# Performance work log

Measured on AMD Instinct MI355X. Metric: run time of the kernel, lower is better.

The kernel has to match this reference:

```python
import jax, jax.numpy as jnp
import numpy as np

HEADS = 12
HEAD_SIZE = 64
NEG = 1e12


def setup_inputs() -> dict:
    key = jax.random.key(0)
    k1, k2 = jax.random.split(key)
    B, L, D = 32, 512, 768
    x = jax.random.normal(k1, (B, L, D), dtype=jnp.float32)
    mask = jnp.ones((B, L), dtype=jnp.float32)  # padding mask (1 = valid)
    W = jax.random.normal(k2, (D, HEADS * HEAD_SIZE * 2), dtype=jnp.float32) * 0.02
    b = jnp.zeros((HEADS * HEAD_SIZE * 2,), dtype=jnp.float32)
    return {"x": x, "mask": mask, "W": W, "b": b}


def _rope_sin_cos(L, s, dtype):
    # bert4keras SinusoidalPositionEmbedding: pe[..., ::2] = sin, pe[..., 1::2] = cos
    pos = jnp.arange(L, dtype=dtype)
    freq = jnp.power(10000.0, -2.0 * jnp.arange(s // 2, dtype=dtype) / s)
    ang = pos[:, None] * freq[None, :]            # [L, s/2]
    sin = jnp.repeat(jnp.sin(ang), 2, axis=-1)    # [L, s]
    cos = jnp.repeat(jnp.cos(ang), 2, axis=-1)    # [L, s]
    return sin, cos


def _rotate_half(t):
    # interleaved rotation: (-t1, t0, -t3, t2, ...)
    t2 = jnp.stack([-t[..., 1::2], t[..., ::2]], axis=-1)
    return t2.reshape(t.shape)


def reference(x, mask, W, b):
    B, L, D = x.shape
    s = HEAD_SIZE
    proj = x @ W + b                               # [B, L, heads*2s]
    proj = proj.reshape(B, L, HEADS, 2 * s)        # split-into-heads + stack
    qw, kw = proj[..., :s], proj[..., s:]
    sin, cos = _rope_sin_cos(L, s, x.dtype)
    sin = sin[None, :, None, :]                    # [1, L, 1, s]
    cos = cos[None, :, None, :]
    qw = qw * cos + _rotate_half(qw) * sin
    kw = kw * cos + _rotate_half(kw) * sin
    logits = jnp.einsum('bmhs,bnhs->bhmn', qw, kw)  # [B, H, L, L]
    m2 = mask[:, None, :, None]
    m3 = mask[:, None, None, :]
    logits = logits * m2 + (1.0 - m2) * -NEG
    logits = logits * m3 + (1.0 - m3) * -NEG
    tril = jnp.tril(jnp.ones((L, L), dtype=logits.dtype), -1)  # strictly lower
    logits = logits - tril * NEG                    # keep upper-triangular spans
    return (logits / jnp.sqrt(jnp.asarray(s, logits.dtype))).reshape(B, HEADS, L * L)
```

## Files before the change

### kernel.cpp

```cpp
#include <hip/hip_runtime.h>
#include <hip/hip_bf16.h>

#define HEADS 12
#define HSIZE 64
#define BATCH 32
#define SEQ 512
#define DIM 768
#define NOUT 1536
#define MROWS 16384
#define NEGV 1e12f

typedef __bf16 bf16x8 __attribute__((ext_vector_type(8)));
typedef float f32x4 __attribute__((ext_vector_type(4)));
typedef unsigned short u16x8 __attribute__((ext_vector_type(8)));
typedef unsigned short u16x4 __attribute__((ext_vector_type(4)));

__device__ __forceinline__ void async16(const void* g, void* l) {
  __builtin_amdgcn_global_load_lds(
      (const __attribute__((address_space(1))) void*)g,
      (__attribute__((address_space(3))) void*)l, 16, 0, 0);
}

__device__ __forceinline__ unsigned short f2b(float f) {
  union { __hip_bfloat16 h; unsigned short u; } cv;
  cv.h = __float2bfloat16(f);
  return cv.u;
}

__global__ void rope_table(float* __restrict__ sin_t, float* __restrict__ cos_t) {
  int idx = blockIdx.x * 256 + threadIdx.x;
  if (idx < SEQ * 32) {
    int pos = idx >> 5;
    int i = idx & 31;
    float freq = powf(10000.0f, -2.0f * (float)i / 64.0f);
    float ang = (float)pos * freq;
    sin_t[idx] = sinf(ang);
    cos_t[idx] = cosf(ang);
  }
}

__global__ void convert_x(const float* __restrict__ x, unsigned short* __restrict__ xb) {
  int idx = blockIdx.x * 256 + threadIdx.x;
  float4 v = ((const float4*)x)[idx];
  ushort4 o;
  o.x = f2b(v.x); o.y = f2b(v.y); o.z = f2b(v.z); o.w = f2b(v.w);
  ((ushort4*)xb)[idx] = o;
}

__global__ void transpose_w(const float* __restrict__ W, unsigned short* __restrict__ Wt) {
  __shared__ unsigned short tile[32][33];
  int n0 = blockIdx.x * 32;
  int k0 = blockIdx.y * 32;
  int tx = threadIdx.x & 31, ty = threadIdx.x >> 5;
#pragma unroll
  for (int j = 0; j < 32; j += 8) {
    tile[ty + j][tx] = f2b(W[(size_t)(k0 + ty + j) * NOUT + n0 + tx]);
  }
  __syncthreads();
#pragma unroll
  for (int j = 0; j < 32; j += 8) {
    Wt[(size_t)(n0 + ty + j) * DIM + k0 + tx] = tile[tx][ty + j];
  }
}

__global__ __launch_bounds__(256) void gemm_rope(
    const unsigned short* __restrict__ xb, const unsigned short* __restrict__ wt,
    const float* __restrict__ bias, const float* __restrict__ sin_t,
    const float* __restrict__ cos_t, unsigned short* __restrict__ q_ws,
    unsigned short* __restrict__ k_ws) {
  __shared__ __align__(16) unsigned short smem[128 * 136];
  unsigned short* As = smem;
  unsigned short* Bs = smem + 4096;
  const int tid = threadIdx.x;
  const int bx = blockIdx.x;
  const int tn = (bx % (NOUT / 128)) * 128;
  const int tm = (bx / (NOUT / 128)) * 128;
  const int wid = tid >> 6, lane = tid & 63;
  const int wm = (wid >> 1) * 64, wn = (wid & 1) * 64;
  const int lrow = lane & 15, lk = (lane >> 4) * 8;

  const int sr = tid >> 2;
  const int sc = (tid & 3) * 8;
  const unsigned short* a_src0 = xb + (size_t)(tm + sr) * DIM + sc;
  const unsigned short* a_src1 = xb + (size_t)(tm + 64 + sr) * DIM + sc;
  const unsigned short* b_src0 = wt + (size_t)(tn + sr) * DIM + sc;
  const unsigned short* b_src1 = wt + (size_t)(tn + 64 + sr) * DIM + sc;
  unsigned short* a_dst0 = &As[tid * 8];
  unsigned short* a_dst1 = &As[2048 + tid * 8];
  unsigned short* b_dst0 = &Bs[tid * 8];
  unsigned short* b_dst1 = &Bs[2048 + tid * 8];

  f32x4 acc[4][4] = {};
  for (int k0 = 0; k0 < DIM; k0 += 32) {
    async16(a_src0 + k0, a_dst0);
    async16(a_src1 + k0, a_dst1);
    async16(b_src0 + k0, b_dst0);
    async16(b_src1 + k0, b_dst1);
    __syncthreads();
    bf16x8 nf[4], mf[4];
#pragma unroll
    for (int i = 0; i < 4; ++i) {
      nf[i] = *(const bf16x8*)&Bs[(wn + i * 16 + lrow) * 32 + lk];
      mf[i] = *(const bf16x8*)&As[(wm + i * 16 + lrow) * 32 + lk];
    }
#pragma unroll
    for (int ai = 0; ai < 4; ++ai)
#pragma unroll
      for (int bi = 0; bi < 4; ++bi)
        acc[ai][bi] = __builtin_amdgcn_mfma_f32_16x16x32_bf16(
            nf[ai], mf[bi], acc[ai][bi], 0, 0, 0);
    __syncthreads();
  }

#pragma unroll
  for (int ai = 0; ai < 4; ++ai) {
    const int nloc = wn + ai * 16 + (lane >> 4) * 4;
    const int colb = tn + nloc;
    const int d0 = colb & 63;
    const float4 b4 = *(const float4*)&bias[colb];
#pragma unroll
    for (int bi = 0; bi < 4; ++bi) {
      const int mloc = wm + bi * 16 + lrow;
      const int pos = (tm + mloc) & (SEQ - 1);
      const float2 s01 = *(const float2*)&sin_t[pos * 32 + (d0 >> 1)];
      const float2 c01 = *(const float2*)&cos_t[pos * 32 + (d0 >> 1)];
      const float v0 = acc[ai][bi][0] + b4.x;
      const float v1 = acc[ai][bi][1] + b4.y;
      const float v2 = acc[ai][bi][2] + b4.z;
      const float v3 = acc[ai][bi][3] + b4.w;
      u16x4 pk;
      pk[0] = f2b(fmaf(v0, c01.x, -v1 * s01.x));
      pk[1] = f2b(fmaf(v1, c01.x,  v0 * s01.x));
      pk[2] = f2b(fmaf(v2, c01.y, -v3 * s01.y));
      pk[3] = f2b(fmaf(v3, c01.y,  v2 * s01.y));
      *(u16x4*)&smem[mloc * 136 + nloc] = pk;
    }
  }
  __syncthreads();

  const int bq = tm >> 9;
  const int pos0 = tm & (SEQ - 1);
  const int head = tn >> 7;
  const size_t rowbase = ((size_t)(bq * HEADS + head) * SEQ + pos0);
  const int rr = tid >> 3;
  const int cc = tid & 7;
#pragma unroll
  for (int p = 0; p < 4; ++p) {
    const int r = p * 32 + rr;
    u16x8 vq = *(const u16x8*)&smem[r * 136 + cc * 8];
    u16x8 vk = *(const u16x8*)&smem[r * 136 + 64 + cc * 8];
    *(u16x8*)&q_ws[(rowbase + r) * 64 + cc * 8] = vq;
    *(u16x8*)&k_ws[(rowbase + r) * 64 + cc * 8] = vk;
  }
}

__global__ __launch_bounds__(256) void qk_kernel(
    const unsigned short* __restrict__ q_ws, const unsigned short* __restrict__ k_ws,
    const float* __restrict__ mask, float* __restrict__ out) {
  __shared__ __align__(16) float ot[128 * 132];
  const int bx = blockIdx.x;
  const int bh = bx >> 4;
  const int t = bx & 15;
  const int tmm = (t >> 2) * 128, tnn = (t & 3) * 128;
  const int bidx = bh / HEADS;
  const int tid = threadIdx.x, wid = tid >> 6, lane = tid & 63;
  const int wm = (wid >> 1) * 64, wn = (wid & 1) * 64;
  const int lrow = lane & 15, lk = (lane >> 4) * 8;
  const unsigned short* Q = q_ws + ((size_t)bh << 15);
  const unsigned short* K = k_ws + ((size_t)bh << 15);

  bf16x8 kf[4][2], qf[4][2];
#pragma unroll
  for (int i = 0; i < 4; ++i) {
#pragma unroll
    for (int ks = 0; ks < 2; ++ks) {
      kf[i][ks] = *(const bf16x8*)&K[(size_t)(tnn + wn + i * 16 + lrow) * 64 + ks * 32 + lk];
      qf[i][ks] = *(const bf16x8*)&Q[(size_t)(tmm + wm + i * 16 + lrow) * 64 + ks * 32 + lk];
    }
  }
  f32x4 acc[4][4] = {};
#pragma unroll
  for (int ai = 0; ai < 4; ++ai)
#pragma unroll
    for (int bi = 0; bi < 4; ++bi) {
      acc[ai][bi] = __builtin_amdgcn_mfma_f32_16x16x32_bf16(kf[ai][0], qf[bi][0], acc[ai][bi], 0, 0, 0);
      acc[ai][bi] = __builtin_amdgcn_mfma_f32_16x16x32_bf16(kf[ai][1], qf[bi][1], acc[ai][bi], 0, 0, 0);
    }

#pragma unroll
  for (int ai = 0; ai < 4; ++ai) {
    const int nloc = wn + ai * 16 + (lane >> 4) * 4;
#pragma unroll
    for (int bi = 0; bi < 4; ++bi) {
      const int mloc = wm + bi * 16 + lrow;
      *(f32x4*)&ot[mloc * 132 + nloc] = acc[ai][bi];
    }
  }
  __syncthreads();

  float* obase = out + ((size_t)bh << 18);
  const float* mrow = mask + (size_t)bidx * SEQ;
  const int cc = tid & 31;
  const int rr = tid >> 5;
  const int n0 = tnn + cc * 4;
  const f32x4 m3v = *(const f32x4*)&mrow[n0];
#pragma unroll
  for (int p = 0; p < 16; ++p) {
    const int r = p * 8 + rr;
    const int m = tmm + r;
    f32x4 v = *(const f32x4*)&ot[r * 132 + cc * 4];
    const float m2 = mrow[m];
    f32x4 o;
#pragma unroll
    for (int j = 0; j < 4; ++j) {
      float vv = v[j];
      vv = vv * m2 + (1.0f - m2) * (-NEGV);
      vv = vv * m3v[j] + (1.0f - m3v[j]) * (-NEGV);
      if (m > n0 + j) vv -= NEGV;
      o[j] = vv * 0.125f;
    }
    __builtin_nontemporal_store(o, (f32x4*)&obase[(size_t)m * 512 + n0]);
  }
}

extern "C" void kernel_launch(void* const* d_in, const int* in_sizes, int n_in,
                              void* d_out, int out_size, void* d_ws, size_t ws_size,
                              hipStream_t stream) {
  const float* x = (const float*)d_in[0];
  const float* mask = (const float*)d_in[1];
  const float* W = (const float*)d_in[2];
  const float* b = (const float*)d_in[3];
  float* out = (float*)d_out;

  char* ws = (char*)d_ws;
  float* sin_t = (float*)(ws + 0);
  float* cos_t = (float*)(ws + 65536);
  unsigned short* xb  = (unsigned short*)(ws + 131072);
  unsigned short* wt  = (unsigned short*)(ws + 25296896);
  unsigned short* q_ws = (unsigned short*)(ws + 27656192);
  unsigned short* k_ws = (unsigned short*)(ws + 52822016);

  rope_table<<<dim3(64), dim3(256), 0, stream>>>(sin_t, cos_t);
  convert_x<<<dim3(MROWS * DIM / 4 / 256), dim3(256), 0, stream>>>(x, xb);
  transpose_w<<<dim3(NOUT / 32, DIM / 32), dim3(256), 0, stream>>>(W, wt);
  gemm_rope<<<dim3((MROWS / 128) * (NOUT / 128)), dim3(256), 0, stream>>>(
      xb, wt, b, sin_t, cos_t, q_ws, k_ws);
  qk_kernel<<<dim3(BATCH * HEADS * 16), dim3(256), 0, stream>>>(q_ws, k_ws, mask, out);
}
```

Baseline: 529.7 us.

## Deepen GEMM K-tile to 64 and loop QK blocks over column tiles

The projection GEMM now stages 64-wide K slices per iteration, which halves the number of barrier-synchronised loop trips and issues more async loads per sync. The QK kernel now launches a quarter as many blocks. Each block keeps its Q fragments in registers and loops over four 128-column K tiles, writing each output tile through a smaller shared-memory staging buffer in two halves. This cuts block launch overhead and redundant Q loads, and the smaller LDS footprint may raise occupancy. The cost is fewer blocks for parallelism, more registers per thread, and extra barriers inside the QK loop.

```diff
diff --git a/kernel.cpp b/kernel.cpp
--- a/kernel.cpp
+++ b/kernel.cpp
@@ -70,7 +70,7 @@
     unsigned short* __restrict__ k_ws) {
   __shared__ __align__(16) unsigned short smem[128 * 136];
   unsigned short* As = smem;
-  unsigned short* Bs = smem + 4096;
+  unsigned short* Bs = smem + 8192;
   const int tid = threadIdx.x;
   const int bx = blockIdx.x;
   const int tn = (bx % (NOUT / 128)) * 128;
@@ -79,36 +79,35 @@
   const int wm = (wid >> 1) * 64, wn = (wid & 1) * 64;
   const int lrow = lane & 15, lk = (lane >> 4) * 8;
 
-  const int sr = tid >> 2;
-  const int sc = (tid & 3) * 8;
-  const unsigned short* a_src0 = xb + (size_t)(tm + sr) * DIM + sc;
-  const unsigned short* a_src1 = xb + (size_t)(tm + 64 + sr) * DIM + sc;
-  const unsigned short* b_src0 = wt + (size_t)(tn + sr) * DIM + sc;
-  const unsigned short* b_src1 = wt + (size_t)(tn + 64 + sr) * DIM + sc;
-  unsigned short* a_dst0 = &As[tid * 8];
-  unsigned short* a_dst1 = &As[2048 + tid * 8];
-  unsigned short* b_dst0 = &Bs[tid * 8];
-  unsigned short* b_dst1 = &Bs[2048 + tid * 8];
+  const int sr = tid >> 3;
+  const int scb = (tid & 7) * 8;
+  const unsigned short* a_src = xb + (size_t)(tm + sr) * DIM + scb;
+  const unsigned short* b_src = wt + (size_t)(tn + sr) * DIM + scb;
 
   f32x4 acc[4][4] = {};
-  for (int k0 = 0; k0 < DIM; k0 += 32) {
-    async16(a_src0 + k0, a_dst0);
-    async16(a_src1 + k0, a_dst1);
-    async16(b_src0 + k0, b_dst0);
-    async16(b_src1 + k0, b_dst1);
+  for (int kt = 0; kt < 12; ++kt) {
+    const int k0 = kt * 64;
+#pragma unroll
+    for (int p = 0; p < 4; ++p) {
+      async16(a_src + (size_t)(p * 32) * DIM + k0, &As[(p * 32 + sr) * 64 + scb]);
+      async16(b_src + (size_t)(p * 32) * DIM + k0, &Bs[(p * 32 + sr) * 64 + scb]);
+    }
     __syncthreads();
-    bf16x8 nf[4], mf[4];
-#pragma unroll
-    for (int i = 0; i < 4; ++i) {
-      nf[i] = *(const bf16x8*)&Bs[(wn + i * 16 + lrow) * 32 + lk];
-      mf[i] = *(const bf16x8*)&As[(wm + i * 16 + lrow) * 32 + lk];
-    }
-#pragma unroll
-    for (int ai = 0; ai < 4; ++ai)
-#pragma unroll
-      for (int bi = 0; bi < 4; ++bi)
-        acc[ai][bi] = __builtin_amdgcn_mfma_f32_16x16x32_bf16(
-            nf[ai], mf[bi], acc[ai][bi], 0, 0, 0);
+#pragma unroll
+    for (int ks = 0; ks < 2; ++ks) {
+      bf16x8 nf[4], mf[4];
+#pragma unroll
+      for (int i = 0; i < 4; ++i) {
+        nf[i] = *(const bf16x8*)&Bs[(wn + i * 16 + lrow) * 64 + ks * 32 + lk];
+        mf[i] = *(const bf16x8*)&As[(wm + i * 16 + lrow) * 64 + ks * 32 + lk];
+      }
+#pragma unroll
+      for (int ai = 0; ai < 4; ++ai)
+#pragma unroll
+        for (int bi = 0; bi < 4; ++bi)
+          acc[ai][bi] = __builtin_amdgcn_mfma_f32_16x16x32_bf16(
+              nf[ai], mf[bi], acc[ai][bi], 0, 0, 0);
+    }
     __syncthreads();
   }
 
@@ -157,69 +156,81 @@
 __global__ __launch_bounds__(256) void qk_kernel(
     const unsigned short* __restrict__ q_ws, const unsigned short* __restrict__ k_ws,
     const float* __restrict__ mask, float* __restrict__ out) {
-  __shared__ __align__(16) float ot[128 * 132];
+  __shared__ __align__(16) float ot[128 * 68];
   const int bx = blockIdx.x;
-  const int bh = bx >> 4;
-  const int t = bx & 15;
-  const int tmm = (t >> 2) * 128, tnn = (t & 3) * 128;
+  const int bh = bx >> 2;
+  const int tmm = (bx & 3) * 128;
   const int bidx = bh / HEADS;
   const int tid = threadIdx.x, wid = tid >> 6, lane = tid & 63;
-  const int wm = (wid >> 1) * 64, wn = (wid & 1) * 64;
+  const int wm = wid * 32;
   const int lrow = lane & 15, lk = (lane >> 4) * 8;
   const unsigned short* Q = q_ws + ((size_t)bh << 15);
   const unsigned short* K = k_ws + ((size_t)bh << 15);
 
-  bf16x8 kf[4][2], qf[4][2];
-#pragma unroll
-  for (int i = 0; i < 4; ++i) {
-#pragma unroll
-    for (int ks = 0; ks < 2; ++ks) {
-      kf[i][ks] = *(const bf16x8*)&K[(size_t)(tnn + wn + i * 16 + lrow) * 64 + ks * 32 + lk];
-      qf[i][ks] = *(const bf16x8*)&Q[(size_t)(tmm + wm + i * 16 + lrow) * 64 + ks * 32 + lk];
-    }
-  }
-  f32x4 acc[4][4] = {};
-#pragma unroll
-  for (int ai = 0; ai < 4; ++ai)
-#pragma unroll
-    for (int bi = 0; bi < 4; ++bi) {
-      acc[ai][bi] = __builtin_amdgcn_mfma_f32_16x16x32_bf16(kf[ai][0], qf[bi][0], acc[ai][bi], 0, 0, 0);
-      acc[ai][bi] = __builtin_amdgcn_mfma_f32_16x16x32_bf16(kf[ai][1], qf[bi][1], acc[ai][bi], 0, 0, 0);
-    }
-
-#pragma unroll
-  for (int ai = 0; ai < 4; ++ai) {
-    const int nloc = wn + ai * 16 + (lane >> 4) * 4;
-#pragma unroll
-    for (int bi = 0; bi < 4; ++bi) {
-      const int mloc = wm + bi * 16 + lrow;
-      *(f32x4*)&ot[mloc * 132 + nloc] = acc[ai][bi];
-    }
-  }
-  __syncthreads();
+  bf16x8 qf[2][2];
+#pragma unroll
+  for (int mi = 0; mi < 2; ++mi)
+#pragma unroll
+    for (int ks = 0; ks < 2; ++ks)
+      qf[mi][ks] = *(const bf16x8*)&Q[(size_t)(tmm + wm + mi * 16 + lrow) * 64 + ks * 32 + lk];
 
   float* obase = out + ((size_t)bh << 18);
   const float* mrow = mask + (size_t)bidx * SEQ;
-  const int cc = tid & 31;
-  const int rr = tid >> 5;
-  const int n0 = tnn + cc * 4;
-  const f32x4 m3v = *(const f32x4*)&mrow[n0];
-#pragma unroll
-  for (int p = 0; p < 16; ++p) {
-    const int r = p * 8 + rr;
-    const int m = tmm + r;
-    f32x4 v = *(const f32x4*)&ot[r * 132 + cc * 4];
-    const float m2 = mrow[m];
-    f32x4 o;
-#pragma unroll
-    for (int j = 0; j < 4; ++j) {
-      float vv = v[j];
-      vv = vv * m2 + (1.0f - m2) * (-NEGV);
-      vv = vv * m3v[j] + (1.0f - m3v[j]) * (-NEGV);
-      if (m > n0 + j) vv -= NEGV;
-      o[j] = vv * 0.125f;
-    }
-    __builtin_nontemporal_store(o, (f32x4*)&obase[(size_t)m * 512 + n0]);
+  const int cc = tid & 15;
+  const int rr = tid >> 4;
+
+  for (int t = 0; t < 4; ++t) {
+    const int tnn = t * 128;
+    bf16x8 kf[8][2];
+#pragma unroll
+    for (int ni = 0; ni < 8; ++ni)
+#pragma unroll
+      for (int ks = 0; ks < 2; ++ks)
+        kf[ni][ks] = *(const bf16x8*)&K[(size_t)(tnn + ni * 16 + lrow) * 64 + ks * 32 + lk];
+
+    f32x4 acc[8][2] = {};
+#pragma unroll
+    for (int ks = 0; ks < 2; ++ks)
+#pragma unroll
+      for (int ni = 0; ni < 8; ++ni)
+#pragma unroll
+        for (int mi = 0; mi < 2; ++mi)
+          acc[ni][mi] = __builtin_amdgcn_mfma_f32_16x16x32_bf16(
+              kf[ni][ks], qf[mi][ks], acc[ni][mi], 0, 0, 0);
+
+#pragma unroll
+    for (int h = 0; h < 2; ++h) {
+      __syncthreads();
+#pragma unroll
+      for (int ai = 0; ai < 4; ++ai) {
+        const int nloc = ai * 16 + (lane >> 4) * 4;
+#pragma unroll
+        for (int mi = 0; mi < 2; ++mi) {
+          const int mloc = wm + mi * 16 + lrow;
+          *(f32x4*)&ot[mloc * 68 + nloc] = acc[h * 4 + ai][mi];
+        }
+      }
+      __syncthreads();
+      const int n0 = tnn + h * 64 + cc * 4;
+      const f32x4 m3v = *(const f32x4*)&mrow[n0];
+#pragma unroll
+      for (int p = 0; p < 8; ++p) {
+        const int r = p * 16 + rr;
+        const int m = tmm + r;
+        f32x4 v = *(const f32x4*)&ot[r * 68 + cc * 4];
+        const float m2 = mrow[m];
+        f32x4 o;
+#pragma unroll
+        for (int j = 0; j < 4; ++j) {
+          float vv = v[j];
+          vv = vv * m2 + (1.0f - m2) * (-NEGV);
+          vv = vv * m3v[j] + (1.0f - m3v[j]) * (-NEGV);
+          if (m > n0 + j) vv -= NEGV;
+          o[j] = vv * 0.125f;
+        }
+        __builtin_nontemporal_store(o, (f32x4*)&obase[(size_t)m * 512 + n0]);
+      }
+    }
   }
 }
 
@@ -245,5 +256,5 @@
   transpose_w<<<dim3(NOUT / 32, DIM / 32), dim3(256), 0, stream>>>(W, wt);
   gemm_rope<<<dim3((MROWS / 128) * (NOUT / 128)), dim3(256), 0, stream>>>(
       xb, wt, b, sin_t, cos_t, q_ws, k_ws);
-  qk_kernel<<<dim3(BATCH * HEADS * 16), dim3(256), 0, stream>>>(q_ws, k_ws, mask, out);
-}
+  qk_kernel<<<dim3(BATCH * HEADS * 4), dim3(256), 0, stream>>>(q_ws, k_ws, mask, out);
+}
```

New measurement: 519.3 us. About the same (-2.0%).
